# Optimization experiments

Hardware: AMD Instinct MI355X
Metric: run time of the kernel (lower is better)

## Reference

```python
import jax, jax.numpy as jnp
import numpy as np

DIM = 1024          # hidden_size
HEADS = 16
KDIM = DIM // 2     # expand_k = 0.5
VDIM = DIM          # expand_v = 1.0
DK = KDIM // HEADS  # 32 head key dim
DV = VDIM // HEADS  # 64 head value dim
LOW = 16            # gate_low_rank_dim
NORMALIZER = 16.0   # gate_logit_normalizer
EPS = 1e-5
B, T = 2, 4096


def setup_inputs() -> dict:
    key = jax.random.key(0)
    ks = jax.random.split(key, 9)
    def lin(k, sh, fan_in):
        return jax.random.normal(k, sh, jnp.float32) * (fan_in ** -0.5)
    return {
        "x":    jax.random.normal(ks[0], (B, T, DIM), jnp.float32),
        "Wq":   lin(ks[1], (DIM, KDIM), DIM),
        "Wk":   lin(ks[2], (DIM, KDIM), DIM),
        "Wv":   lin(ks[3], (DIM, VDIM), DIM),
        "Wgk1": lin(ks[4], (DIM, LOW), DIM),   # low-rank gate proj (no bias)
        "Wgk2": lin(ks[5], (LOW, KDIM), LOW),  # low-rank gate proj (with bias)
        "bgk2": jnp.zeros((KDIM,), jnp.float32),
        "Wg":   lin(ks[6], (DIM, VDIM), DIM),  # output gate proj (no bias)
        "gnw":  jnp.ones((DV,), jnp.float32),  # per-head RMSNorm weight
        "Wo":   lin(ks[7], (VDIM, DIM), VDIM),
    }


def _gla_scan(q, k, v, gk):
    # q,k,gk: (B,T,H,DK)  v: (B,T,H,DV)
    # recurrent form of chunked GLA: h_t = exp(gk_t) (x) h_{t-1} + k_t (outer) v_t
    scale = DK ** -0.5
    def step(h, inp):
        qt, kt, vt, gt = inp                      # (B,H,DK)/(B,H,DV)
        h = h * jnp.exp(gt)[..., None] + kt[..., None] * vt[..., None, :]
        ot = jnp.einsum('bhk,bhkv->bhv', qt * scale, h)
        return h, ot
    h0 = jnp.zeros((q.shape[0], HEADS, DK, DV), q.dtype)
    xs = tuple(jnp.moveaxis(a, 1, 0) for a in (q, k, v, gk))  # time-major
    _, o = jax.lax.scan(step, h0, xs)
    return jnp.moveaxis(o, 0, 1)                  # (B,T,H,DV)


def reference(x, Wq, Wk, Wv, Wgk1, Wgk2, bgk2, Wg, gnw, Wo):
    Bx, Tx, _ = x.shape
    q = (x @ Wq).reshape(Bx, Tx, HEADS, DK)
    k = (x @ Wk).reshape(Bx, Tx, HEADS, DK)
    v = (x @ Wv).reshape(Bx, Tx, HEADS, DV)
    # data-dependent log-decay gate: logsigmoid(low-rank proj) / normalizer
    gk = jax.nn.log_sigmoid((x @ Wgk1) @ Wgk2 + bgk2)
    gk = gk.reshape(Bx, Tx, HEADS, DK) / NORMALIZER
    o = _gla_scan(q, k, v, gk)                    # (B,T,H,DV)
    # fused per-head RMSNorm + swish output gate
    g = (x @ Wg).reshape(Bx, Tx, HEADS, DV)
    o = o * jax.lax.rsqrt(jnp.mean(o * o, axis=-1, keepdims=True) + EPS) * gnw
    o = o * (g * jax.nn.sigmoid(g))
    return o.reshape(Bx, Tx, VDIM) @ Wo
```

## Files before the change

kernel.cpp:

```cpp
#include <hip/hip_runtime.h>

typedef unsigned short u16;
typedef unsigned int u32;
typedef __attribute__((ext_vector_type(8))) short short8;
typedef __attribute__((ext_vector_type(4))) float f32x4;

#define KD 512
#define HEADS 16
#define DK 32
#define DV 64
#define TT 4096
#define MROWS 8192
#define CHUNK 64
#define NCH 64
#define NBH 32
#define QSTR 3328
#define SCALE 0.17677669529663687f

__device__ __forceinline__ u16 f2bf(float f) {
    union { float f; unsigned int u; } x; x.f = f;
    unsigned int u = x.u;
    unsigned int r = (u + 0x7fffu + ((u >> 16) & 1u)) >> 16;
    return (u16)r;
}
__device__ __forceinline__ float bf2f(u16 s) {
    union { unsigned int u; float f; } x; x.u = ((unsigned int)s) << 16;
    return x.f;
}
__device__ __forceinline__ void gload16(const u16* g, u16* l) {
    __builtin_amdgcn_global_load_lds((const __attribute__((address_space(1))) u32*)g,
                                     (__attribute__((address_space(3))) u32*)l, 16, 0, 0);
}

__global__ __launch_bounds__(256) void f32_to_bf16_vec(const float* __restrict__ src,
                                                       u16* __restrict__ dst, int n4) {
    int i = blockIdx.x * 256 + threadIdx.x;
    if (i < n4) {
        const float4 v = ((const float4*)src)[i];
        ushort4 o;
        o.x = f2bf(v.x); o.y = f2bf(v.y); o.z = f2bf(v.z); o.w = f2bf(v.w);
        ((ushort4*)dst)[i] = o;
    }
}

__global__ __launch_bounds__(256) void weight_prep(const float* __restrict__ Wq,
                                                   const float* __restrict__ Wk,
                                                   const float* __restrict__ Wv,
                                                   const float* __restrict__ Wg,
                                                   const float* __restrict__ W1,
                                                   const float* __restrict__ Wo,
                                                   u16* __restrict__ dst) {
    __shared__ float tile[32][33];
    int n0 = blockIdx.x * 32, k0 = blockIdx.y * 32;
    int tx = threadIdx.x & 31, ty = threadIdx.x >> 5;
    int n = n0 + tx;
    const float* src; int sN, cc;
    if (n < 512)       { src = Wq; sN = 512;  cc = n; }
    else if (n < 1024) { src = Wk; sN = 512;  cc = n - 512; }
    else if (n < 2048) { src = Wv; sN = 1024; cc = n - 1024; }
    else if (n < 3072) { src = Wg; sN = 1024; cc = n - 2048; }
    else if (n < 3088) { src = W1; sN = 16;   cc = n - 3072; }
    else if (n < 3328) { src = nullptr; sN = 0; cc = 0; }
    else               { src = Wo; sN = 1024; cc = n - 3328; }
    for (int r = ty; r < 32; r += 8)
        tile[r][tx] = src ? src[(size_t)(k0 + r) * sN + cc] : 0.f;
    __syncthreads();
    for (int r = ty; r < 32; r += 8)
        dst[(size_t)(n0 + r) * 1024 + k0 + tx] = f2bf(tile[tx][r]);
}

#define BARM() do { asm volatile("" ::: "memory"); __builtin_amdgcn_s_barrier(); asm volatile("" ::: "memory"); } while (0)
#define VMW(n) asm volatile("s_waitcnt vmcnt(" #n ")" ::: "memory")

template<int OUTBF>
__global__ __launch_bounds__(512, 2) void gemm8(const u16* __restrict__ A,
                                                const u16* __restrict__ Bt,
                                                void* __restrict__ C,
                                                int M, int N, int K, int nbx) {
    __shared__ u16 SA[2][16384];
    __shared__ u16 SB[2][16384];
    int nwg = gridDim.x, bid = blockIdx.x, cpx = nwg >> 3;
    int wg = (bid & 7) * cpx + (bid >> 3);
    int bx = wg % nbx, by = wg / nbx;
    int brow = by << 8, bcol = bx << 8;
    int tid = threadIdx.x;
    int wv = tid >> 6, lane = tid & 63;
    int wm = wv >> 2, wn = wv & 3;
    int l15 = lane & 15, hi = lane >> 4;
    int rxor = l15 & 7;

    int srw = tid >> 3;
    int sg8 = ((tid & 7) ^ (srw & 7)) << 3;
    const u16* aBase = A + (size_t)(brow + srw) * K + sg8;
    const u16* bBase = Bt + (size_t)(bcol + ((tid >> 8) << 6) + (srw & 31)) * K + sg8;

#define STAGE_A(b, h, tt) do { \
        const u16* s_ = aBase + (size_t)(tt) * 64 + (size_t)(h) * 64 * K; \
        gload16(s_,                    &SA[b][(h) * 8192 + tid * 8]); \
        gload16(s_ + (size_t)128 * K,  &SA[b][(h) * 8192 + 4096 + tid * 8]); \
    } while (0)
#define STAGE_B(b, h, tt) do { \
        const u16* s_ = bBase + (size_t)(tt) * 64 + (size_t)(h) * 32 * K; \
        gload16(s_,                    &SB[b][(h) * 8192 + tid * 8]); \
        gload16(s_ + (size_t)128 * K,  &SB[b][(h) * 8192 + 4096 + tid * 8]); \
    } while (0)

    int aRow = (wm * 64 + l15) * 64;
    int bRow = (wn * 32 + l15) * 64;
    int cg0 = (hi ^ rxor) << 3;
    int cg1 = ((4 + hi) ^ rxor) << 3;

#define READ_A(dst, mh, b) do { \
        _Pragma("unroll") \
        for (int mil_ = 0; mil_ < 4; ++mil_) { \
            dst[mil_ * 2 + 0] = *(const short8*)&SA[b][(mh) * 8192 + mil_ * 1024 + aRow + cg0]; \
            dst[mil_ * 2 + 1] = *(const short8*)&SA[b][(mh) * 8192 + mil_ * 1024 + aRow + cg1]; \
        } } while (0)
#define READ_B(dst, nh, b) do { \
        _Pragma("unroll") \
        for (int nil_ = 0; nil_ < 2; ++nil_) { \
            dst[nil_ * 2 + 0] = *(const short8*)&SB[b][(nh) * 8192 + nil_ * 1024 + bRow + cg0]; \
            dst[nil_ * 2 + 1] = *(const short8*)&SB[b][(nh) * 8192 + nil_ * 1024 + bRow + cg1]; \
        } } while (0)

    f32x4 acc[8][4];
    #pragma unroll
    for (int mi = 0; mi < 8; ++mi)
        #pragma unroll
        for (int ni = 0; ni < 4; ++ni)
            acc[mi][ni] = (f32x4){0.f, 0.f, 0.f, 0.f};

#define MM(mb, nb, AF, BF) do { \
        __builtin_amdgcn_s_setprio(1); \
        _Pragma("unroll") \
        for (int ks_ = 0; ks_ < 2; ++ks_) \
        _Pragma("unroll") \
        for (int mil_ = 0; mil_ < 4; ++mil_) \
        _Pragma("unroll") \
        for (int nil_ = 0; nil_ < 2; ++nil_) \
            acc[(mb) + mil_][(nb) + nil_] = __builtin_amdgcn_mfma_f32_16x16x32_bf16( \
                AF[mil_ * 2 + ks_], BF[nil_ * 2 + ks_], acc[(mb) + mil_][(nb) + nil_], 0, 0, 0); \
        __builtin_amdgcn_s_setprio(0); \
    } while (0)

    int NK = K >> 6, NI = NK >> 1;
    STAGE_B(0, 0, 0); STAGE_A(0, 0, 0); STAGE_A(0, 1, 0); STAGE_B(0, 1, 0);
    STAGE_B(1, 0, 1); STAGE_A(1, 0, 1); STAGE_A(1, 1, 1);
    VMW(6);
    BARM();

    short8 alo[8], ahi[8], bb[4];
    for (int i = 0; i < NI; ++i) {
        int ta = 2 * i + 1; if (ta >= NK) ta = NK - 1;
        int tb = 2 * i + 2; if (tb >= NK) tb = NK - 1;
        int tc = 2 * i + 3; if (tc >= NK) tc = NK - 1;
        STAGE_B(1, 1, ta);
        READ_A(alo, 0, 0); READ_B(bb, 0, 0);
        BARM(); MM(0, 0, alo, bb); BARM();
        STAGE_B(0, 0, tb);
        READ_A(ahi, 1, 0);
        BARM(); MM(4, 0, ahi, bb); BARM();
        STAGE_A(0, 0, tb);
        READ_B(bb, 1, 0);
        BARM(); MM(4, 2, ahi, bb); BARM();
        STAGE_A(0, 1, tb);
        BARM(); MM(0, 2, alo, bb);
        VMW(8);
        BARM();
        STAGE_B(0, 1, tb);
        READ_A(alo, 0, 1); READ_B(bb, 0, 1);
        BARM(); MM(0, 0, alo, bb); BARM();
        STAGE_B(1, 0, tc);
        READ_A(ahi, 1, 1);
        BARM(); MM(4, 0, ahi, bb);
        VMW(10);
        BARM();
        STAGE_A(1, 0, tc);
        READ_B(bb, 1, 1);
        BARM(); MM(4, 2, ahi, bb); BARM();
        STAGE_A(1, 1, tc);
        BARM(); MM(0, 2, alo, bb);
        VMW(6);
        BARM();
    }

    int r0 = brow + wm * 128 + (hi << 2);
    int c0 = bcol + wn * 64 + l15;
    #pragma unroll
    for (int mi = 0; mi < 8; ++mi)
        #pragma unroll
        for (int ni = 0; ni < 4; ++ni)
            #pragma unroll
            for (int rr = 0; rr < 4; ++rr) {
                size_t idx = (size_t)(r0 + mi * 16 + rr) * N + (c0 + ni * 16);
                float val = acc[mi][ni][rr];
                if (OUTBF) ((u16*)C)[idx] = f2bf(val);
                else       ((float*)C)[idx] = val;
            }
#undef STAGE_A
#undef STAGE_B
#undef READ_A
#undef READ_B
#undef MM
}

__device__ __forceinline__ void gate_z8(const u16* __restrict__ xg,
                                        const float* __restrict__ W2,
                                        const float* __restrict__ b2,
                                        int cc, float* out8) {
    short8 x0 = *(const short8*)xg;
    short8 x1 = *(const short8*)(xg + 8);
    float z[8];
    float4 z0 = *(const float4*)(b2 + cc);
    float4 z1 = *(const float4*)(b2 + cc + 4);
    z[0]=z0.x; z[1]=z0.y; z[2]=z0.z; z[3]=z0.w;
    z[4]=z1.x; z[5]=z1.y; z[6]=z1.z; z[7]=z1.w;
    #pragma unroll
    for (int u = 0; u < 16; ++u) {
        float xu = bf2f((u16)(u < 8 ? x0[u] : x1[u - 8]));
        const float4 w0 = *(const float4*)(W2 + (size_t)u * 512 + cc);
        const float4 w1 = *(const float4*)(W2 + (size_t)u * 512 + cc + 4);
        z[0] += xu * w0.x; z[1] += xu * w0.y; z[2] += xu * w0.z; z[3] += xu * w0.w;
        z[4] += xu * w1.x; z[5] += xu * w1.y; z[6] += xu * w1.z; z[7] += xu * w1.w;
    }
    #pragma unroll
    for (int j = 0; j < 8; ++j) {
        float zz = z[j];
        out8[j] = (fminf(zz, 0.f) - log1pf(expf(-fabsf(zz)))) * 0.0625f;
    }
}

__global__ __launch_bounds__(256) void phaseA(const u16* __restrict__ qkvg,
                                              const float* __restrict__ W2,
                                              const float* __restrict__ b2,
                                              float* __restrict__ MT_ws,
                                              float* __restrict__ D_ws) {
    int bh = blockIdx.x >> 6, c = blockIdx.x & 63;
    int b = bh >> 4, h = bh & 15;
    int t0 = b * TT + c * CHUNK;
    __shared__ float gkS[64][36];
    __shared__ u16 kdT_bf[32 * 72];
    __shared__ u16 VT_bf[64 * 72];
    __shared__ float Z[32];
    int tid = threadIdx.x;
    int s = tid >> 2, i0 = (tid & 3) << 3;
    {
        float ls[8];
        gate_z8(qkvg + (size_t)(t0 + s) * QSTR + 3072, W2, b2, h * DK + i0, ls);
        #pragma unroll
        for (int jj = 0; jj < 8; ++jj) gkS[s][i0 + jj] = ls[jj];
    }
    short8 kv = *(const short8*)(qkvg + (size_t)(t0 + s) * QSTR + 512 + h * DK + i0);
    {
        int j0 = (tid & 3) << 4;
        short8 v0 = *(const short8*)(qkvg + (size_t)(t0 + s) * QSTR + 1024 + h * DV + j0);
        short8 v1 = *(const short8*)(qkvg + (size_t)(t0 + s) * QSTR + 1024 + h * DV + j0 + 8);
        #pragma unroll
        for (int jj = 0; jj < 8; ++jj) {
            VT_bf[(j0 + jj) * 72 + s] = (u16)v0[jj];
            VT_bf[(j0 + 8 + jj) * 72 + s] = (u16)v1[jj];
        }
    }
    __syncthreads();
    if (tid < 32) {
        float run = 0.f;
        for (int t = 0; t < 64; ++t) { run += gkS[t][tid]; gkS[t][tid] = run; }
        Z[tid] = run;
    }
    __syncthreads();
    #pragma unroll
    for (int jj = 0; jj < 8; ++jj)
        kdT_bf[(i0 + jj) * 72 + s] = f2bf(expf(Z[i0 + jj] - gkS[s][i0 + jj]) * bf2f((u16)kv[jj]));
    __syncthreads();
    int wave = tid >> 6, lane = tid & 63, l15 = lane & 15, hi = lane >> 4;
    int it = wave & 1, jp = wave >> 1;
    size_t base = ((size_t)(bh * NCH + c)) * 2048;
    #pragma unroll
    for (int jj2 = 0; jj2 < 2; ++jj2) {
        int jt = jp * 2 + jj2;
        f32x4 mc = (f32x4){0.f, 0.f, 0.f, 0.f};
        #pragma unroll
        for (int kc = 0; kc < 2; ++kc) {
            short8 ak = *(const short8*)&kdT_bf[(it * 16 + l15) * 72 + kc * 32 + hi * 8];
            short8 bv = *(const short8*)&VT_bf[(jt * 16 + l15) * 72 + kc * 32 + hi * 8];
            mc = __builtin_amdgcn_mfma_f32_16x16x32_bf16(ak, bv, mc, 0, 0, 0);
        }
        #pragma unroll
        for (int rr = 0; rr < 4; ++rr)
            MT_ws[base + (size_t)(jt * 16 + l15) * 32 + it * 16 + hi * 4 + rr] = mc[rr];
    }
    if (tid < 32) D_ws[(size_t)(bh * NCH + c) * 32 + tid] = expf(Z[tid]);
}

__global__ __launch_bounds__(256) void phaseB(const float* __restrict__ MT_ws,
                                              const float* __restrict__ D_ws,
                                              float* __restrict__ HT_ws) {
    int idx = blockIdx.x * 256 + threadIdx.x;
    int bh = idx >> 11;
    int ji = idx & 2047;
    int i = ji & 31;
    float h = 0.f;
    size_t base = (size_t)bh * NCH * 2048 + ji;
    const float* dp = D_ws + (size_t)bh * NCH * 32 + i;
    for (int c = 0; c < NCH; ++c) {
        HT_ws[base + (size_t)c * 2048] = h;
        h = h * dp[c * 32] + MT_ws[base + (size_t)c * 2048];
    }
}

__global__ __launch_bounds__(256) void phaseC(const u16* __restrict__ qkvg,
                                              const float* __restrict__ W2,
                                              const float* __restrict__ b2,
                                              const float* __restrict__ HT_ws,
                                              const float* __restrict__ gnw,
                                              u16* __restrict__ o_n) {
    int bh = blockIdx.x >> 6, c = blockIdx.x & 63;
    int b = bh >> 4, h = bh & 15;
    int t0 = b * TT + c * CHUNK;
    __shared__ float gkS[64][36];
    __shared__ u16 qh_bf[64 * 40];
    __shared__ u16 kt_bf[64 * 40];
    __shared__ u16 VT_bf[64 * 72];
    __shared__ u16 Ht_bf[64 * 40];
    u16* P_bf = (u16*)&gkS[0][0];
    int tid = threadIdx.x;
    int s = tid >> 2, i0 = (tid & 3) << 3;
    {
        float ls[8];
        gate_z8(qkvg + (size_t)(t0 + s) * QSTR + 3072, W2, b2, h * DK + i0, ls);
        #pragma unroll
        for (int jj = 0; jj < 8; ++jj) gkS[s][i0 + jj] = ls[jj];
    }
    short8 qv = *(const short8*)(qkvg + (size_t)(t0 + s) * QSTR + h * DK + i0);
    short8 kv = *(const short8*)(qkvg + (size_t)(t0 + s) * QSTR + 512 + h * DK + i0);
    {
        int j0 = (tid & 3) << 4;
        short8 v0 = *(const short8*)(qkvg + (size_t)(t0 + s) * QSTR + 1024 + h * DV + j0);
        short8 v1 = *(const short8*)(qkvg + (size_t)(t0 + s) * QSTR + 1024 + h * DV + j0 + 8);
        #pragma unroll
        for (int jj = 0; jj < 8; ++jj) {
            VT_bf[(j0 + jj) * 72 + s] = (u16)v0[jj];
            VT_bf[(j0 + 8 + jj) * 72 + s] = (u16)v1[jj];
        }
    }
    {
        const float* hp = HT_ws + ((size_t)(bh * NCH + c)) * 2048 + tid * 8;
        float4 h0 = *(const float4*)hp;
        float4 h1 = *(const float4*)(hp + 4);
        int j = tid >> 2, ii0 = (tid & 3) << 3;
        ushort4 o0, o1;
        o0.x = f2bf(h0.x); o0.y = f2bf(h0.y); o0.z = f2bf(h0.z); o0.w = f2bf(h0.w);
        o1.x = f2bf(h1.x); o1.y = f2bf(h1.y); o1.z = f2bf(h1.z); o1.w = f2bf(h1.w);
        *(ushort4*)&Ht_bf[j * 40 + ii0] = o0;
        *(ushort4*)&Ht_bf[j * 40 + ii0 + 4] = o1;
    }
    __syncthreads();
    if (tid < 32) {
        float run = 0.f;
        for (int t = 0; t < 64; ++t) { run += gkS[t][tid]; gkS[t][tid] = run; }
    }
    __syncthreads();
    #pragma unroll
    for (int jj = 0; jj < 8; ++jj) {
        float Sv = gkS[s][i0 + jj];
        qh_bf[s * 40 + i0 + jj] = f2bf(bf2f((u16)qv[jj]) * expf(Sv) * SCALE);
        kt_bf[s * 40 + i0 + jj] = f2bf(bf2f((u16)kv[jj]) * expf(fminf(-Sv, 80.f)));
    }
    __syncthreads();
    int wave = tid >> 6, lane = tid & 63, l15 = lane & 15, hi = lane >> 4;
    int w = wave;
    short8 aq = *(const short8*)&qh_bf[(w * 16 + l15) * 40 + hi * 8];
    #pragma unroll
    for (int sn = 0; sn < 4; ++sn) {
        f32x4 sc = (f32x4){0.f, 0.f, 0.f, 0.f};
        if (sn <= w) {
            short8 bk = *(const short8*)&kt_bf[(sn * 16 + l15) * 40 + hi * 8];
            sc = __builtin_amdgcn_mfma_f32_16x16x32_bf16(aq, bk, sc, 0, 0, 0);
        }
        #pragma unroll
        for (int rr = 0; rr < 4; ++rr) {
            float val = sc[rr];
            if (sn > w || (sn == w && l15 > hi * 4 + rr)) val = 0.f;
            P_bf[(w * 16 + hi * 4 + rr) * 72 + sn * 16 + l15] = f2bf(val);
        }
    }
    __syncthreads();
    f32x4 acc[4];
    #pragma unroll
    for (int jn = 0; jn < 4; ++jn) {
        f32x4 a = (f32x4){0.f, 0.f, 0.f, 0.f};
        short8 bhf = *(const short8*)&Ht_bf[(jn * 16 + l15) * 40 + hi * 8];
        acc[jn] = __builtin_amdgcn_mfma_f32_16x16x32_bf16(aq, bhf, a, 0, 0, 0);
    }
    int nkc = (w < 2) ? 1 : 2;
    for (int kc = 0; kc < nkc; ++kc) {
        short8 ap = *(const short8*)&P_bf[(w * 16 + l15) * 72 + kc * 32 + hi * 8];
        #pragma unroll
        for (int jn = 0; jn < 4; ++jn) {
            short8 bv = *(const short8*)&VT_bf[(jn * 16 + l15) * 72 + kc * 32 + hi * 8];
            acc[jn] = __builtin_amdgcn_mfma_f32_16x16x32_bf16(ap, bv, acc[jn], 0, 0, 0);
        }
    }
    #pragma unroll
    for (int rr = 0; rr < 4; ++rr) {
        float sum2 = 0.f;
        #pragma unroll
        for (int jn = 0; jn < 4; ++jn) sum2 += acc[jn][rr] * acc[jn][rr];
        sum2 += __shfl_xor(sum2, 1);
        sum2 += __shfl_xor(sum2, 2);
        sum2 += __shfl_xor(sum2, 4);
        sum2 += __shfl_xor(sum2, 8);
        float rms = rsqrtf(sum2 * (1.f / 64.f) + 1e-5f);
        int t = w * 16 + hi * 4 + rr;
        #pragma unroll
        for (int jn = 0; jn < 4; ++jn) {
            int j = jn * 16 + l15;
            float g = bf2f(qkvg[(size_t)(t0 + t) * QSTR + 2048 + h * DV + j]);
            float sw = g / (1.f + expf(-g));
            float o = acc[jn][rr] * rms * gnw[j] * sw;
            o_n[(size_t)(t0 + t) * 1024 + h * DV + j] = f2bf(o);
        }
    }
}

extern "C" void kernel_launch(void* const* d_in, const int* in_sizes, int n_in,
                              void* d_out, int out_size, void* d_ws, size_t ws_size,
                              hipStream_t stream) {
    const float* x    = (const float*)d_in[0];
    const float* Wq   = (const float*)d_in[1];
    const float* Wk   = (const float*)d_in[2];
    const float* Wv   = (const float*)d_in[3];
    const float* Wgk1 = (const float*)d_in[4];
    const float* Wgk2 = (const float*)d_in[5];
    const float* bgk2 = (const float*)d_in[6];
    const float* Wg   = (const float*)d_in[7];
    const float* gnw  = (const float*)d_in[8];
    const float* Wo   = (const float*)d_in[9];

    char* ws = (char*)d_ws;
    size_t off = 0;
    u16* xb      = (u16*)(ws + off); off += (size_t)MROWS * 1024 * 2;
    u16* Wall    = (u16*)(ws + off); off += (size_t)4352 * 1024 * 2;
    u16* qkvg    = (u16*)(ws + off); off += (size_t)MROWS * QSTR * 2;
    float* MT_ws = (float*)(ws + off); off += (size_t)NBH * NCH * 2048 * 4;
    float* D_ws  = (float*)(ws + off); off += (size_t)NBH * NCH * 32 * 4;
    float* HT_ws = (float*)(ws + off); off += (size_t)NBH * NCH * 2048 * 4;
    u16* o_n     = (u16*)(ws + off); off += (size_t)MROWS * 1024 * 2;
    u16* WcatT   = Wall;
    u16* WoT     = Wall + (size_t)3328 * 1024;

    f32_to_bf16_vec<<<MROWS, 256, 0, stream>>>(x, xb, MROWS * 1024 / 4);
    weight_prep<<<dim3(136, 32), 256, 0, stream>>>(Wq, Wk, Wv, Wg, Wgk1, Wo, Wall);
    gemm8<1><<<416, 512, 0, stream>>>(xb, WcatT, qkvg, MROWS, QSTR, 1024, 13);
    phaseA<<<NBH * NCH, 256, 0, stream>>>(qkvg, Wgk2, bgk2, MT_ws, D_ws);
    phaseB<<<256, 256, 0, stream>>>(MT_ws, D_ws, HT_ws);
    phaseC<<<NBH * NCH, 256, 0, stream>>>(qkvg, Wgk2, bgk2, HT_ws, gnw, o_n);
    gemm8<0><<<128, 512, 0, stream>>>(o_n, WoT, d_out, MROWS, 1024, 1024, 4);
}
```

Before: 181.0 us.

## Use smaller-tile GEMM for output projection and merge staging phases in gemm8

```diff
diff --git a/kernel.cpp b/kernel.cpp
--- a/kernel.cpp
+++ b/kernel.cpp
@@ -160,11 +160,9 @@
         STAGE_B(0, 0, tb);
         READ_A(ahi, 1, 0);
         BARM(); MM(4, 0, ahi, bb); BARM();
-        STAGE_A(0, 0, tb);
+        STAGE_A(0, 0, tb); STAGE_A(0, 1, tb);
         READ_B(bb, 1, 0);
-        BARM(); MM(4, 2, ahi, bb); BARM();
-        STAGE_A(0, 1, tb);
-        BARM(); MM(0, 2, alo, bb);
+        BARM(); MM(4, 2, ahi, bb); MM(0, 2, alo, bb);
         VMW(8);
         BARM();
         STAGE_B(0, 1, tb);
@@ -175,11 +173,9 @@
         BARM(); MM(4, 0, ahi, bb);
         VMW(10);
         BARM();
-        STAGE_A(1, 0, tc);
+        STAGE_A(1, 0, tc); STAGE_A(1, 1, tc);
         READ_B(bb, 1, 1);
-        BARM(); MM(4, 2, ahi, bb); BARM();
-        STAGE_A(1, 1, tc);
-        BARM(); MM(0, 2, alo, bb);
+        BARM(); MM(4, 2, ahi, bb); MM(0, 2, alo, bb);
         VMW(6);
         BARM();
     }
@@ -202,6 +198,74 @@
 #undef READ_A
 #undef READ_B
 #undef MM
+}
+
+template<int OUTBF>
+__global__ __launch_bounds__(256) void gemm_sb(const u16* __restrict__ A,
+                                               const u16* __restrict__ Bt,
+                                               void* __restrict__ C,
+                                               int M, int N, int K, int nbx) {
+    __shared__ u16 As[128 * 64];
+    __shared__ u16 Bs[128 * 64];
+    int nwg = gridDim.x;
+    int bid = blockIdx.x;
+    int cpx = nwg >> 3;
+    int wg = (bid & 7) * cpx + (bid >> 3);
+    int bx = wg % nbx, by = wg / nbx;
+    int tid = threadIdx.x;
+    int wave = tid >> 6, lane = tid & 63;
+    int wr = wave >> 1, wc = wave & 1;
+    int brow = by * 128, bcol = bx * 128;
+    int srow = tid >> 3;
+    int sgrp = (tid & 7) ^ (srow & 7);
+    const u16* aS = A + (size_t)(brow + srow) * K + sgrp * 8;
+    const u16* bS = Bt + (size_t)(bcol + srow) * K + sgrp * 8;
+    f32x4 acc[4][4];
+    #pragma unroll
+    for (int mi = 0; mi < 4; ++mi)
+        #pragma unroll
+        for (int ni = 0; ni < 4; ++ni)
+            acc[mi][ni] = (f32x4){0.f, 0.f, 0.f, 0.f};
+    int l15 = lane & 15, hi = lane >> 4;
+    int rxor = l15 & 7;
+    for (int kt = 0; kt < K; kt += 64) {
+        __syncthreads();
+        #pragma unroll
+        for (int i_ = 0; i_ < 4; ++i_) {
+            gload16(aS + (size_t)i_ * 32 * K + kt, As + tid * 8 + i_ * 2048);
+            gload16(bS + (size_t)i_ * 32 * K + kt, Bs + tid * 8 + i_ * 2048);
+        }
+        __syncthreads();
+        #pragma unroll
+        for (int ks = 0; ks < 2; ++ks) {
+            short8 af[4], bfr[4];
+            int g = ks * 4 + hi;
+            #pragma unroll
+            for (int i = 0; i < 4; ++i)
+                af[i] = *(const short8*)(As + (size_t)(wr * 64 + i * 16 + l15) * 64 + ((g ^ rxor) << 3));
+            #pragma unroll
+            for (int i = 0; i < 4; ++i)
+                bfr[i] = *(const short8*)(Bs + (size_t)(wc * 64 + i * 16 + l15) * 64 + ((g ^ rxor) << 3));
+            #pragma unroll
+            for (int mi = 0; mi < 4; ++mi)
+                #pragma unroll
+                for (int ni = 0; ni < 4; ++ni)
+                    acc[mi][ni] = __builtin_amdgcn_mfma_f32_16x16x32_bf16(af[mi], bfr[ni], acc[mi][ni], 0, 0, 0);
+        }
+    }
+    int r0 = brow + wr * 64 + (hi << 2);
+    int c0 = bcol + wc * 64 + l15;
+    #pragma unroll
+    for (int mi = 0; mi < 4; ++mi)
+        #pragma unroll
+        for (int ni = 0; ni < 4; ++ni)
+            #pragma unroll
+            for (int rr = 0; rr < 4; ++rr) {
+                size_t idx = (size_t)(r0 + mi * 16 + rr) * N + (c0 + ni * 16);
+                float val = acc[mi][ni][rr];
+                if (OUTBF) ((u16*)C)[idx] = f2bf(val);
+                else       ((float*)C)[idx] = val;
+            }
 }
 
 __device__ __forceinline__ void gate_z8(const u16* __restrict__ xg,
@@ -455,5 +519,5 @@
     phaseA<<<NBH * NCH, 256, 0, stream>>>(qkvg, Wgk2, bgk2, MT_ws, D_ws);
     phaseB<<<256, 256, 0, stream>>>(MT_ws, D_ws, HT_ws);
     phaseC<<<NBH * NCH, 256, 0, stream>>>(qkvg, Wgk2, bgk2, HT_ws, gnw, o_n);
-    gemm8<0><<<128, 512, 0, stream>>>(o_n, WoT, d_out, MROWS, 1024, 1024, 4);
-}
+    gemm_sb<0><<<8 * 64, 256, 0, stream>>>(o_n, WoT, d_out, MROWS, 1024, 1024, 8);
+}
```

Measured after the change: 174.0 us. 3.8% less time.
